# Kernel tuning notes

Hardware: AMD Instinct MI355X
Metric: run time of the kernel (lower is better)

## Reference

```python
import jax, jax.numpy as jnp
import numpy as np

B, NPG, K, H, G, L = 8, 128, 64, 600, 50, 6
N = B * NPG
CUTOFF = 10.0
BOX = 20.0
NUM_Z = 100


def setup_inputs() -> dict:
    key = jax.random.key(0)
    ks = jax.random.split(key, 16)
    s = 0.05
    z = jax.random.randint(ks[0], (N,), 0, 85)
    pos = jax.random.uniform(ks[1], (N, 3), dtype=jnp.float32) * BOX
    # weights stored as [in, out] (transposed torch Linear) so x @ w applies directly
    inp = {
        "z": z,
        "pos": pos,
        "embedding": jax.random.normal(ks[2], (NUM_Z, H), jnp.float32) * s,
        "mlp_w1": jax.random.normal(ks[3], (L, G, H), jnp.float32) * s,
        "mlp_b1": jnp.zeros((L, H), jnp.float32),
        "mlp_w2": jax.random.normal(ks[4], (L, H, H), jnp.float32) * s,
        "mlp_b2": jnp.zeros((L, H), jnp.float32),
        "lin1_w": jax.random.normal(ks[5], (L, H, H), jnp.float32) * s,  # CFConv lin1, no bias
        "lin2_w": jax.random.normal(ks[6], (L, H, H), jnp.float32) * s,
        "lin2_b": jnp.zeros((L, H), jnp.float32),
        "int_lin_w": jax.random.normal(ks[7], (L, H, H), jnp.float32) * s,
        "int_lin_b": jnp.zeros((L, H), jnp.float32),
        "pool_w": jax.random.normal(ks[8], (H, H), jnp.float32) * s,
        "pool_b": jnp.zeros((H,), jnp.float32),
    }
    return inp


def _ssp(x):
    # shifted softplus used by SchNet
    return jax.nn.softplus(x) - jnp.log(2.0)


def _build_graph(pos):
    # radius graph within each of the B graphs, capped at K neighbors per node
    posg = pos.reshape(B, NPG, 3)
    diff = posg[:, :, None, :] - posg[:, None, :, :]          # [B,n,n,3]
    dist2 = jnp.sum(diff * diff, axis=-1)                     # [B,n,n]
    eye = jnp.eye(NPG, dtype=bool)
    ok = (dist2 <= CUTOFF * CUTOFF) & (~eye)[None]
    neg = jnp.where(ok, -dist2, -jnp.inf)
    vals, idx = jax.lax.top_k(neg, K)                         # nearest K in-radius
    valid = jnp.isfinite(vals)                                # [B,n,K]
    nbr = idx + (jnp.arange(B) * NPG)[:, None, None]          # global node ids
    # recompute distances from gathered positions (differentiable, safe at masked slots)
    pos_nbr = pos[nbr.reshape(-1)].reshape(B, NPG, K, 3)
    dvec = posg[:, :, None, :] - pos_nbr
    dsq = jnp.sum(dvec * dvec, axis=-1)
    d = jnp.sqrt(jnp.where(valid, dsq, 1.0))
    d = jnp.where(valid, d, 0.0)                              # [B,n,K]
    return nbr, d, valid.astype(pos.dtype)


def reference(pos, embedding, mlp_w1, mlp_b1, mlp_w2, mlp_b2, lin1_w, lin2_w,
              lin2_b, int_lin_w, int_lin_b, pool_w, pool_b, z):
    nbr, d, valid = _build_graph(pos)
    nbr_flat = nbr.reshape(-1)

    # Gaussian smearing
    offs = jnp.linspace(0.0, CUTOFF, G)
    coeff = -0.5 / (offs[1] - offs[0]) ** 2
    edge_attr = jnp.exp(coeff * (d[..., None] - offs) ** 2)   # [B,n,K,G]
    # cosine cutoff, zero for invalid (padded) edges
    C = 0.5 * (jnp.cos(d * jnp.pi / CUTOFF) + 1.0) * valid    # [B,n,K]

    h = embedding[z]                                          # [N,H]
    for l in range(L):
        Wf = _ssp(edge_attr @ mlp_w1[l] + mlp_b1[l]) @ mlp_w2[l] + mlp_b2[l]
        Wf = Wf * C[..., None]                                # [B,n,K,H]
        x1 = h @ lin1_w[l]                                    # [N,H]
        xj = x1[nbr_flat].reshape(B, NPG, K, H)               # gather neighbors
        msg = jnp.sum(xj * Wf, axis=2).reshape(N, H)          # aggregate (add)
        m = msg @ lin2_w[l] + lin2_b[l]
        m = _ssp(m)
        m = m @ int_lin_w[l] + int_lin_b[l]
        h = h + m

    pooled = h.reshape(B, NPG, H).mean(axis=1)                # mean pool per graph
    return pooled @ pool_w + pool_b                           # [B, emb_dim]
```

## Files before the change

### kernel.cpp

```cpp
#include <hip/hip_runtime.h>
#include <cmath>

#define NB   8
#define NPG  128
#define NN   1024
#define KNB  64
#define HD   600
#define GG   50
#define LL   6
#define EE   (NN*KNB)
#define WROW 640
#define WCOL 608
#define NKNOT 1024

typedef __attribute__((ext_vector_type(8))) short short8;
typedef __attribute__((ext_vector_type(4))) short short4v;
typedef __attribute__((ext_vector_type(4))) float f32x4;

__device__ __forceinline__ short f2b(float f) {
  union { float f; unsigned u; } v; v.f = f;
  unsigned u = v.u;
  u += 0x7fffu + ((u >> 16) & 1u);
  return (short)(u >> 16);
}

__device__ __forceinline__ float b2f(unsigned us) {
  union { unsigned u; float f; } v; v.u = us << 16; return v.f;
}

__device__ __forceinline__ float ssp_fast(float x) {
  return fmaxf(x, 0.0f) + __logf(1.0f + __expf(-fabsf(x))) - 0.69314718055994531f;
}

__global__ __launch_bounds__(128) void build_graph_k(const float* __restrict__ pos,
        int* __restrict__ nbr, float* __restrict__ dist, float* __restrict__ cval) {
#pragma clang fp contract(off)
  __shared__ float d2s[128];
  __shared__ int scnt;
  int i = blockIdx.x;
  int li = i & 127;
  int base = i - li;
  int j = threadIdx.x;
  if (j == 0) scnt = 0;
  float px = pos[3*i], py = pos[3*i+1], pz = pos[3*i+2];
  int gj = base + j;
  float dx = px - pos[3*gj], dy = py - pos[3*gj+1], dz = pz - pos[3*gj+2];
  float d2 = dx*dx + dy*dy + dz*dz;
  bool valid = (j != li) && (d2 <= 100.0f);
  d2s[j] = valid ? d2 : 3.0e38f;
  __syncthreads();
  if (valid) {
    atomicAdd(&scnt, 1);
    int rank = 0;
    for (int j2 = 0; j2 < 128; ++j2) {
      float o = d2s[j2];
      rank += (o < d2 || (o == d2 && j2 < j)) ? 1 : 0;
    }
    if (rank < KNB) {
      int e = i*KNB + rank;
      nbr[e] = gj;
      float d = sqrtf(d2);
      dist[e] = d;
      cval[e] = 0.5f * (cosf(d * 0.31415926535897931f) + 1.0f);
    }
  }
  __syncthreads();
  int cnt = scnt; if (cnt > KNB) cnt = KNB;
  if (j < KNB && j >= cnt) {
    int e = i*KNB + j;
    nbr[e] = i; dist[e] = 0.0f; cval[e] = 0.0f;
  }
}

__global__ __launch_bounds__(256) void prep_k(const float* __restrict__ w1,
    short* __restrict__ basis, short* __restrict__ w1b) {
  int idx = blockIdx.x*256 + threadIdx.x;
  if (idx < NKNOT*64) {
    int i = idx >> 6, g = idx & 63;
    float v = 0.0f;
    if (g < GG) {
      const float step = 10.0f/49.0f;
      const float coeff = -0.5f/(step*step);
      float d = (float)i * (10.0f/(float)(NKNOT-1));
      float dd = d - step*(float)g;
      v = __expf(coeff*dd*dd);
    }
    basis[idx] = f2b(v);
  } else {
    int r = idx - NKNOT*64;
    if (r >= LL*WROW*64) return;
    int l = r / (WROW*64); int rem = r - l*WROW*64;
    int n = rem >> 6, k = rem & 63;
    float v = (n < HD && k < GG) ? w1[(size_t)l*GG*HD + (size_t)k*HD + n] : 0.0f;
    w1b[r] = f2b(v);
  }
}

__global__ __launch_bounds__(256) void conv_all_k(const float* __restrict__ l1w,
    const float* __restrict__ l2w, const float* __restrict__ ilw,
    const float* __restrict__ w2, short* __restrict__ dst) {
  __shared__ float T[64][65];
  int w = blockIdx.x;
  int kind = w / 6, l = w - kind*6;
  const float* s = (kind == 0) ? l1w : (kind == 1) ? l2w : (kind == 2) ? ilw : w2;
  s += (size_t)l*360000;
  int n0 = blockIdx.y*64, k0 = blockIdx.z*64;
  int tid = threadIdx.x;
  int ta = tid & 63, tb = tid >> 6;
  #pragma unroll
  for (int p = 0; p < 16; ++p) {
    int k = k0 + p*4 + tb;
    int n = n0 + ta;
    T[p*4 + tb][ta] = (k < HD && n < HD) ? s[(size_t)k*HD + n] : 0.0f;
  }
  __syncthreads();
  #pragma unroll
  for (int p = 0; p < 16; ++p) {
    int n = n0 + p*4 + tb;
    int k = k0 + ta;
    if (k < WCOL)
      dst[(size_t)w*WROW*WCOL + (size_t)n*WCOL + k] = f2b(T[ta][p*4 + tb]);
  }
}

__global__ __launch_bounds__(256) void embed_k(const int* __restrict__ z,
        const float* __restrict__ emb, float* __restrict__ h, short* __restrict__ hb) {
  int i = blockIdx.x;
  int zi = z[i];
  for (int j = threadIdx.x; j < WCOL; j += 256) {
    float v = (j < HD) ? emb[(size_t)zi*HD + j] : 0.0f;
    if (j < HD) h[(size_t)i*HD + j] = v;
    hb[(size_t)i*WCOL + j] = f2b(v);
  }
}

__global__ __launch_bounds__(256) void tabA_k(const short* __restrict__ basis,
    const short* __restrict__ w1b, const float* __restrict__ b1all,
    short* __restrict__ ttab_all) {
  const int MT = NKNOT/128;
  int l = blockIdx.x / MT;
  int mb = blockIdx.x - l*MT;
  const short* Bw = w1b + (size_t)l*WROW*64;
  short* outb = ttab_all + (size_t)l*NKNOT*WCOL;
  __shared__ __align__(16) short As[128*40];
  __shared__ __align__(16) short Bs[128*40];
  int tid = threadIdx.x;
  int lane = tid & 63, wv = tid >> 6;
  int wr = wv >> 1, wc = wv & 1;
  int col = lane & 15, quad = lane >> 4;
  int m0 = mb * 128;
  int n0 = blockIdx.y * 128;
  f32x4 acc[4][4] = {};
  for (int k0 = 0; k0 < 64; k0 += 32) {
    #pragma unroll
    for (int rep = 0; rep < 2; ++rep) {
      int s = tid + rep*256;
      int row = s >> 2, seg = s & 3;
      *(short8*)&As[row*40 + seg*8] =
          *(const short8*)(basis + (size_t)(m0 + row)*64 + k0 + seg*8);
      *(short8*)&Bs[row*40 + seg*8] =
          *(const short8*)(Bw + (size_t)(n0 + row)*64 + k0 + seg*8);
    }
    __syncthreads();
    short8 af[4], bf[4];
    #pragma unroll
    for (int mt = 0; mt < 4; ++mt)
      af[mt] = *(const short8*)&As[(wr*64 + mt*16 + col)*40 + quad*8];
    #pragma unroll
    for (int jt = 0; jt < 4; ++jt)
      bf[jt] = *(const short8*)&Bs[(wc*64 + jt*16 + col)*40 + quad*8];
    #pragma unroll
    for (int mt = 0; mt < 4; ++mt)
      #pragma unroll
      for (int jt = 0; jt < 4; ++jt)
        acc[mt][jt] = __builtin_amdgcn_mfma_f32_16x16x32_bf16(af[mt], bf[jt], acc[mt][jt], 0, 0, 0);
    __syncthreads();
  }
  #pragma unroll
  for (int jt = 0; jt < 4; ++jt) {
    int j = n0 + wc*64 + jt*16 + col;
    if (j >= WCOL) continue;
    float bj = (j < HD) ? b1all[(size_t)l*HD + j] : 0.0f;
    #pragma unroll
    for (int mt = 0; mt < 4; ++mt)
      #pragma unroll
      for (int r = 0; r < 4; ++r) {
        int row = m0 + wr*64 + mt*16 + quad*4 + r;
        short v = (j < HD) ? f2b(ssp_fast(acc[mt][jt][r] + bj)) : (short)0;
        outb[(size_t)row*WCOL + j] = v;
      }
  }
}

__global__ __launch_bounds__(256) void tabB_k(const short* __restrict__ ttab_all,
    const short* __restrict__ nwall, const float* __restrict__ b2all,
    short* __restrict__ wtab_b) {
  const int MT = NKNOT/128;
  int l = blockIdx.x / MT;
  int mb = blockIdx.x - l*MT;
  const short* A  = ttab_all + (size_t)l*NKNOT*WCOL;
  const short* Bw = nwall + (size_t)(18 + l)*WROW*WCOL;
  short* P = wtab_b + (size_t)l*NKNOT*HD;
  __shared__ __align__(16) short As[128*40];
  __shared__ __align__(16) short Bs[128*40];
  int tid = threadIdx.x;
  int lane = tid & 63, wv = tid >> 6;
  int wr = wv >> 1, wc = wv & 1;
  int col = lane & 15, quad = lane >> 4;
  int m0 = mb * 128;
  int n0 = blockIdx.y * 128;
  f32x4 acc[4][4] = {};
  for (int k0 = 0; k0 < WCOL; k0 += 32) {
    #pragma unroll
    for (int rep = 0; rep < 2; ++rep) {
      int s = tid + rep*256;
      int row = s >> 2, seg = s & 3;
      *(short8*)&As[row*40 + seg*8] =
          *(const short8*)(A + (size_t)(m0 + row)*WCOL + k0 + seg*8);
      *(short8*)&Bs[row*40 + seg*8] =
          *(const short8*)(Bw + (size_t)(n0 + row)*WCOL + k0 + seg*8);
    }
    __syncthreads();
    short8 af[4], bf[4];
    #pragma unroll
    for (int mt = 0; mt < 4; ++mt)
      af[mt] = *(const short8*)&As[(wr*64 + mt*16 + col)*40 + quad*8];
    #pragma unroll
    for (int jt = 0; jt < 4; ++jt)
      bf[jt] = *(const short8*)&Bs[(wc*64 + jt*16 + col)*40 + quad*8];
    #pragma unroll
    for (int mt = 0; mt < 4; ++mt)
      #pragma unroll
      for (int jt = 0; jt < 4; ++jt)
        acc[mt][jt] = __builtin_amdgcn_mfma_f32_16x16x32_bf16(af[mt], bf[jt], acc[mt][jt], 0, 0, 0);
    __syncthreads();
  }
  #pragma unroll
  for (int jt = 0; jt < 4; ++jt) {
    int j = n0 + wc*64 + jt*16 + col;
    if (j >= HD) continue;
    float bj = b2all[(size_t)l*HD + j];
    #pragma unroll
    for (int mt = 0; mt < 4; ++mt)
      #pragma unroll
      for (int r = 0; r < 4; ++r) {
        int row = m0 + wr*64 + mt*16 + quad*4 + r;
        P[(size_t)row*HD + j] = f2b(acc[mt][jt][r] + bj);
      }
  }
}

__global__ __launch_bounds__(192) void gather_k(const short* __restrict__ tabb,
    const float* __restrict__ cval, const int* __restrict__ nbr,
    const float* __restrict__ dist, const short* __restrict__ x1b,
    short* __restrict__ msgb) {
  __shared__ float cvs[64];
  __shared__ int nbs[64];
  __shared__ int tix[64];
  __shared__ float tfr[64];
  int node = blockIdx.x, tid = threadIdx.x;
  if (tid < 64) {
    int e = node*KNB + tid;
    cvs[tid] = cval[e];
    nbs[tid] = nbr[e];
    float u = dist[e] * ((float)(NKNOT-1)/10.0f);
    int i = (int)u;
    if (i > NKNOT-2) i = NKNOT-2;
    tix[tid] = i;
    tfr[tid] = u - (float)i;
  }
  __syncthreads();
  int j = tid*4;
  if (j >= WCOL) return;
  if (j >= HD) {
    *(uint2*)&msgb[(size_t)node*WCOL + j] = make_uint2(0u, 0u);
    return;
  }
  float s[4] = {0.f, 0.f, 0.f, 0.f};
  #pragma unroll 4
  for (int e = 0; e < KNB; ++e) {
    float Ce = cvs[e];
    if (Ce == 0.0f) continue;
    const short* w0 = tabb + (size_t)tix[e]*HD + j;
    float f = tfr[e];
    uint2 wa = *(const uint2*)w0;
    uint2 wb = *(const uint2*)(w0 + HD);
    uint2 xv = *(const uint2*)(x1b + (size_t)nbs[e]*WCOL + j);
    float a0 = b2f(wa.x & 0xffffu), a1 = b2f(wa.x >> 16);
    float a2 = b2f(wa.y & 0xffffu), a3 = b2f(wa.y >> 16);
    float b0 = b2f(wb.x & 0xffffu), b1 = b2f(wb.x >> 16);
    float b2v = b2f(wb.y & 0xffffu), b3 = b2f(wb.y >> 16);
    float x0 = b2f(xv.x & 0xffffu), x1v = b2f(xv.x >> 16);
    float x2 = b2f(xv.y & 0xffffu), x3 = b2f(xv.y >> 16);
    s[0] += Ce * (a0 + f*(b0 - a0)) * x0;
    s[1] += Ce * (a1 + f*(b1 - a1)) * x1v;
    s[2] += Ce * (a2 + f*(b2v - a2)) * x2;
    s[3] += Ce * (a3 + f*(b3 - a3)) * x3;
  }
  uint2 pack;
  pack.x = (unsigned)(unsigned short)f2b(s[0]) | ((unsigned)(unsigned short)f2b(s[1]) << 16);
  pack.y = (unsigned)(unsigned short)f2b(s[2]) | ((unsigned)(unsigned short)f2b(s[3]) << 16);
  *(uint2*)&msgb[(size_t)node*WCOL + j] = pack;
}

template<int MODE>
__global__ __launch_bounds__(256) void gemm_node_k(
    const short* __restrict__ A, const short* __restrict__ Bw,
    const float* __restrict__ bias, float* __restrict__ outf,
    short* __restrict__ outb, float* __restrict__ hacc) {
  __shared__ __align__(16) short As[2][32*40];
  __shared__ __align__(16) short Bs[2][64*40];
  int tid = threadIdx.x;
  int lane = tid & 63, wv = tid >> 6;
  int col = lane & 15, quad = lane >> 4;
  int m0 = blockIdx.x * 32;
  int n0 = blockIdx.y * 64;
  int ar = tid >> 3, aseg = tid & 7;
  int br = tid >> 2, bseg = tid & 3;
  const short* Aptr = A  + (size_t)(m0 + ar)*WCOL + aseg*4;
  const short* Bptr = Bw + (size_t)(n0 + br)*WCOL + bseg*8;
  f32x4 acc[2] = {};
  {
    short4v a0 = *(const short4v*)Aptr;
    short8  b0 = *(const short8*)Bptr;
    *(short4v*)&As[0][ar*40 + aseg*4] = a0;
    *(short8*)&Bs[0][br*40 + bseg*8] = b0;
  }
  __syncthreads();
  for (int kk = 0; kk < 19; ++kk) {
    int cur = kk & 1, nxt = cur ^ 1;
    short4v a_n; short8 b_n;
    if (kk < 18) {
      a_n = *(const short4v*)(Aptr + (kk + 1)*32);
      b_n = *(const short8*) (Bptr + (kk + 1)*32);
    }
    short8 bf = *(const short8*)&Bs[cur][(wv*16 + col)*40 + quad*8];
    #pragma unroll
    for (int mt = 0; mt < 2; ++mt) {
      short8 af = *(const short8*)&As[cur][(mt*16 + col)*40 + quad*8];
      acc[mt] = __builtin_amdgcn_mfma_f32_16x16x32_bf16(af, bf, acc[mt], 0, 0, 0);
    }
    if (kk < 18) {
      *(short4v*)&As[nxt][ar*40 + aseg*4] = a_n;
      *(short8*)&Bs[nxt][br*40 + bseg*8] = b_n;
    }
    __syncthreads();
  }
  int j = n0 + wv*16 + col;
  if (MODE == 0) {
    if (j < WCOL) {
      #pragma unroll
      for (int mt = 0; mt < 2; ++mt)
        #pragma unroll
        for (int r = 0; r < 4; ++r) {
          int row = m0 + mt*16 + quad*4 + r;
          outb[(size_t)row*WCOL + j] = (j < HD) ? f2b(acc[mt][r]) : (short)0;
        }
    }
  } else if (MODE == 1) {
    if (j < WCOL) {
      float bj = (j < HD) ? bias[j] : 0.0f;
      #pragma unroll
      for (int mt = 0; mt < 2; ++mt)
        #pragma unroll
        for (int r = 0; r < 4; ++r) {
          int row = m0 + mt*16 + quad*4 + r;
          outb[(size_t)row*WCOL + j] = (j < HD) ? f2b(ssp_fast(acc[mt][r] + bj)) : (short)0;
        }
    }
  } else {
    if (j < WCOL) {
      #pragma unroll
      for (int mt = 0; mt < 2; ++mt)
        #pragma unroll
        for (int r = 0; r < 4; ++r) {
          int row = m0 + mt*16 + quad*4 + r;
          if (j < HD) {
            float nv = hacc[(size_t)row*HD + j] + acc[mt][r] + bias[j];
            hacc[(size_t)row*HD + j] = nv;
            outb[(size_t)row*WCOL + j] = f2b(nv);
          } else {
            outb[(size_t)row*WCOL + j] = 0;
          }
        }
    }
  }
}

__global__ __launch_bounds__(256) void pool_mean_k(const float* __restrict__ h,
                                                   float* __restrict__ pooled) {
  int b = blockIdx.x;
  int c = blockIdx.y*256 + threadIdx.x;
  if (c >= HD) return;
  float s = 0.0f;
  for (int n = 0; n < NPG; ++n) s += h[(size_t)(b*NPG + n)*HD + c];
  pooled[(size_t)b*HD + c] = s * (1.0f/128.0f);
}

__global__ __launch_bounds__(256) void pool_out_k(const float* __restrict__ pooled,
    const float* __restrict__ pw, const float* __restrict__ pb,
    float* __restrict__ out) {
  __shared__ float red[4][64];
  int b = blockIdx.y;
  int tid = threadIdx.x;
  int jl = tid & 63, q = tid >> 6;
  int j = blockIdx.x*64 + jl;
  float s = 0.0f;
  if (j < HD) {
    int c0 = q*150, c1 = c0 + 150;
    for (int c = c0; c < c1; ++c)
      s += pooled[(size_t)b*HD + c] * pw[(size_t)c*HD + j];
  }
  red[q][jl] = s;
  __syncthreads();
  if (q == 0 && j < HD)
    out[(size_t)b*HD + j] = red[0][jl] + red[1][jl] + red[2][jl] + red[3][jl] + pb[j];
}

extern "C" void kernel_launch(void* const* d_in, const int* in_sizes, int n_in,
                              void* d_out, int out_size, void* d_ws, size_t ws_size,
                              hipStream_t stream) {
  const int*   z    = (const int*)d_in[0];
  const float* pos  = (const float*)d_in[1];
  const float* emb  = (const float*)d_in[2];
  const float* w1   = (const float*)d_in[3];
  const float* b1   = (const float*)d_in[4];
  const float* w2   = (const float*)d_in[5];
  const float* b2   = (const float*)d_in[6];
  const float* l1w  = (const float*)d_in[7];
  const float* l2w  = (const float*)d_in[8];
  const float* l2b  = (const float*)d_in[9];
  const float* ilw  = (const float*)d_in[10];
  const float* ilb  = (const float*)d_in[11];
  const float* pw   = (const float*)d_in[12];
  const float* pb   = (const float*)d_in[13];
  float* ws = (float*)d_ws;
  int*   nbr   = (int*)ws;
  float* cv    = ws + 65536;
  float* dist  = ws + 131072;
  float* pooled= ws + 196608;
  float* h     = ws + 204800;
  short* h_b   = (short*)(ws + 819200);
  short* msg_b = (short*)(ws + 1130496);
  short* mtmp_b= (short*)(ws + 1441792);
  short* x1_b  = (short*)(ws + 1753088);
  short* basis = (short*)(ws + 2064384);
  short* ttab  = (short*)(ws + 2097152);
  short* wtab_b= (short*)(ws + 3964928);
  short* w1b   = (short*)(ws + 5808128);
  short* nwall = (short*)(ws + 5931008);
  float* out   = (float*)d_out;

  const size_t WSZ = (size_t)WROW*WCOL;

  build_graph_k<<<NN, 128, 0, stream>>>(pos, nbr, dist, cv);
  prep_k<<<(NKNOT*64 + LL*WROW*64 + 255)/256, 256, 0, stream>>>(w1, basis, w1b);
  conv_all_k<<<dim3(24, 10, 10), 256, 0, stream>>>(l1w, l2w, ilw, w2, nwall);
  embed_k<<<NN, 256, 0, stream>>>(z, emb, h, h_b);

  tabA_k<<<dim3(LL*(NKNOT/128), 5), 256, 0, stream>>>(basis, w1b, b1, ttab);
  tabB_k<<<dim3(LL*(NKNOT/128), 5), 256, 0, stream>>>(ttab, nwall, b2, wtab_b);

  dim3 gn(32, 10);
  for (int l = 0; l < LL; ++l) {
    gemm_node_k<0><<<gn, 256, 0, stream>>>(h_b, nwall + (size_t)(0*6 + l)*WSZ,
        nullptr, nullptr, x1_b, nullptr);
    gather_k<<<NN, 192, 0, stream>>>(wtab_b + (size_t)l*NKNOT*HD, cv, nbr, dist, x1_b, msg_b);
    gemm_node_k<1><<<gn, 256, 0, stream>>>(msg_b, nwall + (size_t)(1*6 + l)*WSZ,
        l2b + (size_t)l*HD, nullptr, mtmp_b, nullptr);
    gemm_node_k<2><<<gn, 256, 0, stream>>>(mtmp_b, nwall + (size_t)(2*6 + l)*WSZ,
        ilb + (size_t)l*HD, nullptr, h_b, h);
  }
  pool_mean_k<<<dim3(NB, 3), 256, 0, stream>>>(h, pooled);
  pool_out_k<<<dim3(10, NB), 256, 0, stream>>>(pooled, pw, pb, out);
}
```

Before: 493.2 us.

## Split-K node GEMMs across two thread groups and fuse pooling kernels

Each node GEMM block now runs 512 threads as two 256-thread groups. Each group handles half of the K dimension (10 and 9 stages), and the partial accumulators are reduced through shared memory. This halves the serial K-loop length per block, because the grid of 320 blocks was too small to hide latency. Mean pooling and the output projection are also merged into one kernel, which removes a launch at the cost of recomputing the mean in each of the 10 column blocks.

```diff
diff --git a/kernel.cpp b/kernel.cpp
--- a/kernel.cpp
+++ b/kernel.cpp
@@ -304,48 +304,65 @@
 }
 
 template<int MODE>
-__global__ __launch_bounds__(256) void gemm_node_k(
+__global__ __launch_bounds__(512) void gemm_node_k(
     const short* __restrict__ A, const short* __restrict__ Bw,
     const float* __restrict__ bias, float* __restrict__ outf,
     short* __restrict__ outb, float* __restrict__ hacc) {
-  __shared__ __align__(16) short As[2][32*40];
-  __shared__ __align__(16) short Bs[2][64*40];
+  __shared__ __align__(16) short As[2][2][32*40];
+  __shared__ __align__(16) short Bs[2][2][64*40];
+  __shared__ __align__(16) float red[256*8];
   int tid = threadIdx.x;
-  int lane = tid & 63, wv = tid >> 6;
+  int g = tid >> 8;
+  int t = tid & 255;
+  int lane = t & 63, wv = t >> 6;
   int col = lane & 15, quad = lane >> 4;
   int m0 = blockIdx.x * 32;
   int n0 = blockIdx.y * 64;
-  int ar = tid >> 3, aseg = tid & 7;
-  int br = tid >> 2, bseg = tid & 3;
-  const short* Aptr = A  + (size_t)(m0 + ar)*WCOL + aseg*4;
-  const short* Bptr = Bw + (size_t)(n0 + br)*WCOL + bseg*8;
+  int ar = t >> 3, aseg = t & 7;
+  int br = t >> 2, bseg = t & 3;
+  const int NST = g ? 9 : 10;
+  const int kb  = g ? 320 : 0;
+  const short* Aptr = A  + (size_t)(m0 + ar)*WCOL + kb + aseg*4;
+  const short* Bptr = Bw + (size_t)(n0 + br)*WCOL + kb + bseg*8;
   f32x4 acc[2] = {};
   {
     short4v a0 = *(const short4v*)Aptr;
     short8  b0 = *(const short8*)Bptr;
-    *(short4v*)&As[0][ar*40 + aseg*4] = a0;
-    *(short8*)&Bs[0][br*40 + bseg*8] = b0;
-  }
-  __syncthreads();
-  for (int kk = 0; kk < 19; ++kk) {
+    *(short4v*)&As[g][0][ar*40 + aseg*4] = a0;
+    *(short8*)&Bs[g][0][br*40 + bseg*8] = b0;
+  }
+  __syncthreads();
+  for (int kk = 0; kk < 10; ++kk) {
     int cur = kk & 1, nxt = cur ^ 1;
     short4v a_n; short8 b_n;
-    if (kk < 18) {
+    if (kk + 1 < NST) {
       a_n = *(const short4v*)(Aptr + (kk + 1)*32);
       b_n = *(const short8*) (Bptr + (kk + 1)*32);
     }
-    short8 bf = *(const short8*)&Bs[cur][(wv*16 + col)*40 + quad*8];
-    #pragma unroll
-    for (int mt = 0; mt < 2; ++mt) {
-      short8 af = *(const short8*)&As[cur][(mt*16 + col)*40 + quad*8];
-      acc[mt] = __builtin_amdgcn_mfma_f32_16x16x32_bf16(af, bf, acc[mt], 0, 0, 0);
-    }
-    if (kk < 18) {
-      *(short4v*)&As[nxt][ar*40 + aseg*4] = a_n;
-      *(short8*)&Bs[nxt][br*40 + bseg*8] = b_n;
+    if (kk < NST) {
+      short8 bf = *(const short8*)&Bs[g][cur][(wv*16 + col)*40 + quad*8];
+      #pragma unroll
+      for (int mt = 0; mt < 2; ++mt) {
+        short8 af = *(const short8*)&As[g][cur][(mt*16 + col)*40 + quad*8];
+        acc[mt] = __builtin_amdgcn_mfma_f32_16x16x32_bf16(af, bf, acc[mt], 0, 0, 0);
+      }
+    }
+    if (kk + 1 < NST) {
+      *(short4v*)&As[g][nxt][ar*40 + aseg*4] = a_n;
+      *(short8*)&Bs[g][nxt][br*40 + bseg*8] = b_n;
     }
     __syncthreads();
   }
+  if (g) {
+    #pragma unroll
+    for (int mt = 0; mt < 2; ++mt)
+      *(f32x4*)&red[(t*2 + mt)*4] = acc[mt];
+  }
+  __syncthreads();
+  if (g) return;
+  #pragma unroll
+  for (int mt = 0; mt < 2; ++mt)
+    acc[mt] += *(const f32x4*)&red[(t*2 + mt)*4];
   int j = n0 + wv*16 + col;
   if (MODE == 0) {
     if (j < WCOL) {
@@ -387,29 +404,26 @@
   }
 }
 
-__global__ __launch_bounds__(256) void pool_mean_k(const float* __restrict__ h,
-                                                   float* __restrict__ pooled) {
-  int b = blockIdx.x;
-  int c = blockIdx.y*256 + threadIdx.x;
-  if (c >= HD) return;
-  float s = 0.0f;
-  for (int n = 0; n < NPG; ++n) s += h[(size_t)(b*NPG + n)*HD + c];
-  pooled[(size_t)b*HD + c] = s * (1.0f/128.0f);
-}
-
-__global__ __launch_bounds__(256) void pool_out_k(const float* __restrict__ pooled,
+__global__ __launch_bounds__(256) void pool_fused_k(const float* __restrict__ h,
     const float* __restrict__ pw, const float* __restrict__ pb,
     float* __restrict__ out) {
+  __shared__ float ps[HD];
   __shared__ float red[4][64];
   int b = blockIdx.y;
   int tid = threadIdx.x;
+  for (int c = tid; c < HD; c += 256) {
+    float s = 0.0f;
+    for (int n = 0; n < NPG; ++n) s += h[(size_t)(b*NPG + n)*HD + c];
+    ps[c] = s * (1.0f/128.0f);
+  }
+  __syncthreads();
   int jl = tid & 63, q = tid >> 6;
   int j = blockIdx.x*64 + jl;
   float s = 0.0f;
   if (j < HD) {
     int c0 = q*150, c1 = c0 + 150;
     for (int c = c0; c < c1; ++c)
-      s += pooled[(size_t)b*HD + c] * pw[(size_t)c*HD + j];
+      s += ps[c] * pw[(size_t)c*HD + j];
   }
   red[q][jl] = s;
   __syncthreads();
@@ -450,6 +464,7 @@
   short* w1b   = (short*)(ws + 5808128);
   short* nwall = (short*)(ws + 5931008);
   float* out   = (float*)d_out;
+  (void)pooled;
 
   const size_t WSZ = (size_t)WROW*WCOL;
 
@@ -463,14 +478,13 @@
 
   dim3 gn(32, 10);
   for (int l = 0; l < LL; ++l) {
-    gemm_node_k<0><<<gn, 256, 0, stream>>>(h_b, nwall + (size_t)(0*6 + l)*WSZ,
+    gemm_node_k<0><<<gn, 512, 0, stream>>>(h_b, nwall + (size_t)(0*6 + l)*WSZ,
         nullptr, nullptr, x1_b, nullptr);
     gather_k<<<NN, 192, 0, stream>>>(wtab_b + (size_t)l*NKNOT*HD, cv, nbr, dist, x1_b, msg_b);
-    gemm_node_k<1><<<gn, 256, 0, stream>>>(msg_b, nwall + (size_t)(1*6 + l)*WSZ,
+    gemm_node_k<1><<<gn, 512, 0, stream>>>(msg_b, nwall + (size_t)(1*6 + l)*WSZ,
         l2b + (size_t)l*HD, nullptr, mtmp_b, nullptr);
-    gemm_node_k<2><<<gn, 256, 0, stream>>>(mtmp_b, nwall + (size_t)(2*6 + l)*WSZ,
+    gemm_node_k<2><<<gn, 512, 0, stream>>>(mtmp_b, nwall + (size_t)(2*6 + l)*WSZ,
         ilb + (size_t)l*HD, nullptr, h_b, h);
   }
-  pool_mean_k<<<dim3(NB, 3), 256, 0, stream>>>(h, pooled);
-  pool_out_k<<<dim3(10, NB), 256, 0, stream>>>(pooled, pw, pb, out);
-}
+  pool_fused_k<<<dim3(10, NB), 256, 0, stream>>>(h, pw, pb, out);
+}
```

After: 471.6 us. 1.05x faster.
